# Kernel optimization log

Measured on AMD Instinct MI355X. Metric: run time of the kernel, lower is better.

## Reference

```python
import jax, jax.numpy as jnp
import numpy as np

NUM_HEADS = 4
LN_EPS = 1e-5


def setup_inputs() -> dict:
    key = jax.random.key(0)
    B, S, D = 4, 2048, 1024
    H = NUM_HEADS
    hd = D // H
    ks = jax.random.split(key, 8)
    s = 1.0 / np.sqrt(hd)
    inp = {
        "embeddings": jax.random.normal(ks[0], (B, S, D), dtype=jnp.float32),
        # per-head Q/K/V projection weights (torch Linear weight layout [out,in])
        "Wq": jax.random.normal(ks[1], (H, hd, hd), dtype=jnp.float32) * s,
        "Wk": jax.random.normal(ks[2], (H, hd, hd), dtype=jnp.float32) * s,
        "Wv": jax.random.normal(ks[3], (H, hd, hd), dtype=jnp.float32) * s,
        # lens bias scalars: causal, intent, temporal, normative (init values from module)
        "bias_scalars": jnp.array([0.1, 0.15, 0.05, 0.2], dtype=jnp.float32),
        "Wo_w": jax.random.normal(ks[4], (D, D), dtype=jnp.float32) / np.sqrt(D),
        "Wo_b": jnp.zeros((D,), dtype=jnp.float32),
        "ln_g": jnp.ones((D,), dtype=jnp.float32),
        "ln_b": jnp.zeros((D,), dtype=jnp.float32),
    }
    return inp


def _legal_biases(x, bias_scalars):
    """x: [B,H,S,hd] per-head embeddings. Returns stacked bias [B,H,S,S]."""
    B, H, S, hd = x.shape
    # head 0: CAUSAL -> strictly upper triangular mask * causal_bias
    causal = jnp.triu(jnp.ones((S, S), dtype=x.dtype), k=1)  # [S,S]
    b0 = causal[None] * bias_scalars[0]                      # [1,S,S] -> bcast B
    b0 = jnp.broadcast_to(b0, (B, S, S))
    # head 1: INTENTIONALITY -> outer product of embedding norms, global-mean threshold
    mag1 = jnp.linalg.norm(x[:, 1], axis=-1)                 # [B,S]
    intent = mag1[:, :, None] * mag1[:, None, :]             # [B,S,S]
    b1 = (intent > intent.mean()).astype(x.dtype) * bias_scalars[1]
    # head 2: TEMPORAL -> exp(-|i-j|/S)
    pos = jnp.arange(S, dtype=x.dtype)
    prox = jnp.exp(-jnp.abs(pos[:, None] - pos[None, :]) / S)  # [S,S]
    b2 = jnp.broadcast_to(prox[None] * bias_scalars[2], (B, S, S))
    # head 3: NORMATIVE -> outer product of last feature, > 0.5 threshold
    v3 = x[:, 3, :, -1]                                      # [B,S]
    viol = v3[:, :, None] * v3[:, None, :]                   # [B,S,S]
    b3 = (viol > 0.5).astype(x.dtype) * bias_scalars[3]
    return jnp.stack([b0, b1, b2, b3], axis=1)               # [B,H,S,S]


def _forward(embeddings, Wq, Wk, Wv, bias_scalars, Wo_w, Wo_b, ln_g, ln_b):
    B, S, D = embeddings.shape
    H = NUM_HEADS
    hd = D // H
    x = embeddings.reshape(B, S, H, hd).transpose(0, 2, 1, 3)     # [B,H,S,hd]
    # torch Linear: y = x @ W.T
    Q = jnp.einsum('bhsd,hed->bhse', x, Wq)
    K = jnp.einsum('bhsd,hed->bhse', x, Wk)
    V = jnp.einsum('bhsd,hed->bhse', x, Wv)
    scores = jnp.einsum('bhse,bhte->bhst', Q, K) / np.sqrt(hd)    # [B,H,S,S]
    scores = scores + _legal_biases(x, bias_scalars)
    weights = jax.nn.softmax(scores, axis=-1)                     # [B,H,S,S]
    attended = jnp.einsum('bhst,bhte->bhse', weights, V)          # [B,H,S,hd]
    concat = attended.transpose(0, 2, 1, 3).reshape(B, S, D)      # head order = concat order
    out = concat @ Wo_w.T + Wo_b
    # layer_norm(out + embeddings)
    y = out + embeddings
    mu = y.mean(axis=-1, keepdims=True)
    var = ((y - mu) ** 2).mean(axis=-1, keepdims=True)
    output = (y - mu) / jnp.sqrt(var + LN_EPS) * ln_g + ln_b      # [B,S,D]
    average_weights = weights.mean(axis=1)                        # [B,S,S]
    guilt = jax.nn.softmax(average_weights.sum(axis=-1), axis=-1) # [B,S]
    return output, average_weights, guilt


def reference(embeddings, Wq, Wk, Wv, bias_scalars, Wo_w, Wo_b, ln_g, ln_b):
    return _forward(embeddings, Wq, Wk, Wv, bias_scalars, Wo_w, Wo_b, ln_g, ln_b)
```

## Files before the change

kernel.cpp:

```cpp
#include <hip/hip_runtime.h>
#include <hip/hip_bf16.h>
#include <math.h>

#define S_ 2048
#define D_ 1024
#define H_ 4
#define HD_ 256
#define B_ 4

typedef __hip_bfloat16 bf16;
typedef short s16x8 __attribute__((ext_vector_type(8)));
typedef float f32x4 __attribute__((ext_vector_type(4)));

#define GLOAD16(g, l)                                             \
    __builtin_amdgcn_global_load_lds(                             \
        (const __attribute__((address_space(1))) void*)(g),       \
        (__attribute__((address_space(3))) void*)(l), 16, 0, 0)


template <int MODE>
__global__ __launch_bounds__(256) void mfma_nt(
    int K,
    const bf16* __restrict__ A, int lda, long sA_b, long sA_h,
    const bf16* __restrict__ Bm, int ldb, long sB_b, long sB_h,
    void* __restrict__ Cp, int ldc, long sC_b, long sC_h,
    int zdiv, int bbase,
    const double* __restrict__ mag1d, const double* __restrict__ v3d,
    const double* __restrict__ meand, const float* __restrict__ bias_sc)
{
    __shared__ __align__(16) short As[128 * 32];
    __shared__ __align__(16) short Bs[128 * 32];

    const int tid = threadIdx.x;
    const int w = tid >> 6, lane = tid & 63;
    const int srow = lane >> 2;
    const int scol = (((lane & 3) ^ (srow & 3)) << 3);
    const int quad = lane >> 4, r = lane & 15;
    const int qx = quad ^ (r & 3);
    const int wr = (w >> 1) * 64, wc = (w & 1) * 64;
    const int zb = blockIdx.z / zdiv, zh = blockIdx.z % zdiv;

    const bf16* Ap = A + (size_t)zb * sA_b + (size_t)zh * sA_h +
                     (size_t)blockIdx.y * 128 * lda;
    const bf16* Bp = Bm + (size_t)zb * sB_b + (size_t)zh * sB_h +
                     (size_t)blockIdx.x * 128 * ldb;

    f32x4 acc[4][4] = {};

    for (int k0 = 0; k0 < K; k0 += 32) {
        if (k0) __syncthreads();
#pragma unroll
        for (int l = 0; l < 2; l++) {
            GLOAD16(Ap + (size_t)(w * 32 + l * 16 + srow) * lda + (k0 + scol),
                    &As[(w * 32 + l * 16) * 32]);
            GLOAD16(Bp + (size_t)(w * 32 + l * 16 + srow) * ldb + (k0 + scol),
                    &Bs[(w * 32 + l * 16) * 32]);
        }
        __syncthreads();

        s16x8 af[4], bfv[4];
        const s16x8* A8 = (const s16x8*)As;
        const s16x8* B8 = (const s16x8*)Bs;
#pragma unroll
        for (int i = 0; i < 4; i++) af[i] = A8[(wr + i * 16 + r) * 4 + qx];
#pragma unroll
        for (int j = 0; j < 4; j++) bfv[j] = B8[(wc + j * 16 + r) * 4 + qx];
#pragma unroll
        for (int i = 0; i < 4; i++)
#pragma unroll
            for (int j = 0; j < 4; j++)
                acc[i][j] = __builtin_amdgcn_mfma_f32_16x16x32_bf16(
                    af[i], bfv[j], acc[i][j], 0, 0, 0);
    }

    const int row0 = blockIdx.y * 128 + wr + quad * 4;
    const int col0 = blockIdx.x * 128 + wc + r;

    if (MODE == 0) {
        float* C = (float*)Cp + (size_t)zb * sC_b + (size_t)zh * sC_h;
#pragma unroll
        for (int i = 0; i < 4; i++)
#pragma unroll
            for (int j = 0; j < 4; j++)
#pragma unroll
                for (int p = 0; p < 4; p++)
                    C[(size_t)(row0 + i * 16 + p) * ldc + (col0 + j * 16)] = acc[i][j][p];
    } else if (MODE == 1) {
        bf16* C = (bf16*)Cp + (size_t)zb * sC_b + (size_t)zh * sC_h;
#pragma unroll
        for (int i = 0; i < 4; i++)
#pragma unroll
            for (int j = 0; j < 4; j++)
#pragma unroll
                for (int p = 0; p < 4; p++)
                    C[(size_t)(row0 + i * 16 + p) * ldc + (col0 + j * 16)] =
                        __float2bfloat16(acc[i][j][p]);
    } else {
        float* C = (float*)Cp + (size_t)zb * sC_b + (size_t)zh * sC_h;
        const int h = zh;
        const int bbatch = bbase + zb;
        const float bsc = bias_sc[h];
        if (h == 0) {
#pragma unroll
            for (int i = 0; i < 4; i++)
#pragma unroll
                for (int j = 0; j < 4; j++)
#pragma unroll
                    for (int p = 0; p < 4; p++) {
                        const int rr = row0 + i * 16 + p, c = col0 + j * 16;
                        C[(size_t)rr * ldc + c] = acc[i][j][p] + ((c > rr) ? bsc : 0.0f);
                    }
        } else if (h == 2) {
#pragma unroll
            for (int i = 0; i < 4; i++)
#pragma unroll
                for (int j = 0; j < 4; j++)
#pragma unroll
                    for (int p = 0; p < 4; p++) {
                        const int rr = row0 + i * 16 + p, c = col0 + j * 16;
                        int d = c - rr; d = d < 0 ? -d : d;
                        C[(size_t)rr * ldc + c] =
                            acc[i][j][p] + bsc * expf(-(float)d * (1.0f / 2048.0f));
                    }
        } else {
            const double* src = (h == 1) ? mag1d : v3d;
            const double thr = (h == 1) ? meand[0] : 0.5;
            double rv[16], cv[4];
#pragma unroll
            for (int i = 0; i < 4; i++)
#pragma unroll
                for (int p = 0; p < 4; p++)
                    rv[i * 4 + p] = src[(size_t)bbatch * S_ + row0 + i * 16 + p];
#pragma unroll
            for (int j = 0; j < 4; j++)
                cv[j] = src[(size_t)bbatch * S_ + col0 + j * 16];
#pragma unroll
            for (int i = 0; i < 4; i++)
#pragma unroll
                for (int j = 0; j < 4; j++)
#pragma unroll
                    for (int p = 0; p < 4; p++) {
                        const int rr = row0 + i * 16 + p, c = col0 + j * 16;
                        C[(size_t)rr * ldc + c] =
                            acc[i][j][p] + ((rv[i * 4 + p] * cv[j] > thr) ? bsc : 0.0f);
                    }
        }
    }
}

__global__ __launch_bounds__(512) void mfma_pv(const bf16* __restrict__ Pm,
                                               const bf16* __restrict__ Vt,
                                               bf16* __restrict__ Cc) {
    __shared__ __align__(16) short L[6][12288];

    const int tid = threadIdx.x;
    const int w = tid >> 6, lane = tid & 63;
    const int quad = lane >> 4, r = lane & 15;
    const int qx = quad ^ (r & 3);
    const int wr = (w >> 2) * 64, wc = (w & 3) * 64;

    const int bid = blockIdx.x;
    const int bh = (bid & 7) * 2 + ((bid >> 3) >> 4);
    const int rb = (bid >> 3) & 15;
    const int b = bh >> 2, h = bh & 3;

    const bf16* Ap = Pm + ((size_t)bh * S_ + (size_t)rb * 128) * S_;
    const bf16* Bp = Vt + (size_t)(h * B_ + b) * HD_ * S_;

    const int srow = tid >> 2;
    const int scol = (((tid & 3) ^ (srow & 3)) << 3);
    const int wbase = w * 512;

    f32x4 acc[4][4] = {};

    auto stage = [&](int bs, int t) {
        short* sb = &L[bs][0];
        const int k0 = t * 32;
        GLOAD16(Ap + (size_t)srow * S_ + (k0 + scol), sb + wbase);
        GLOAD16(Bp + (size_t)srow * S_ + (k0 + scol), sb + 4096 + wbase);
        GLOAD16(Bp + (size_t)(128 + srow) * S_ + (k0 + scol), sb + 8192 + wbase);
    };
    auto compute = [&](int bs) {
        const s16x8* A8 = (const s16x8*)&L[bs][0];
        const s16x8* B8 = (const s16x8*)&L[bs][4096];
        s16x8 af[4], bfv[4];
#pragma unroll
        for (int i = 0; i < 4; i++) af[i] = A8[(wr + i * 16 + r) * 4 + qx];
#pragma unroll
        for (int j = 0; j < 4; j++) bfv[j] = B8[(wc + j * 16 + r) * 4 + qx];
        __builtin_amdgcn_s_setprio(1);
#pragma unroll
        for (int i = 0; i < 4; i++)
#pragma unroll
            for (int j = 0; j < 4; j++)
                acc[i][j] = __builtin_amdgcn_mfma_f32_16x16x32_bf16(
                    af[i], bfv[j], acc[i][j], 0, 0, 0);
        __builtin_amdgcn_s_setprio(0);
    };

#define PV_WAITB(N)                                           \
    asm volatile("s_waitcnt vmcnt(" #N ")" ::: "memory");     \
    __builtin_amdgcn_s_barrier();                             \
    __builtin_amdgcn_sched_barrier(0);

    stage(0, 0); stage(1, 1); stage(2, 2); stage(3, 3); stage(4, 4);

    int cb = 0, sn = 5;
#pragma unroll 1
    for (int t = 0; t < 59; ++t) {
        PV_WAITB(12);
        stage(sn, t + 5);
        compute(cb);
        cb = (cb == 5) ? 0 : cb + 1;
        sn = (sn == 5) ? 0 : sn + 1;
    }
    PV_WAITB(12); compute(cb); cb = (cb == 5) ? 0 : cb + 1;
    PV_WAITB(9);  compute(cb); cb = (cb == 5) ? 0 : cb + 1;
    PV_WAITB(6);  compute(cb); cb = (cb == 5) ? 0 : cb + 1;
    PV_WAITB(3);  compute(cb); cb = (cb == 5) ? 0 : cb + 1;
    PV_WAITB(0);  compute(cb);
#undef PV_WAITB

    const int row0 = rb * 128 + wr + quad * 4;
    const int col0 = h * HD_ + wc + r;
    bf16* C = Cc + (size_t)b * S_ * D_;
#pragma unroll
    for (int i = 0; i < 4; i++)
#pragma unroll
        for (int j = 0; j < 4; j++)
#pragma unroll
            for (int p = 0; p < 4; p++)
                C[(size_t)(row0 + i * 16 + p) * D_ + col0 + j * 16] =
                    __float2bfloat16(acc[i][j][p]);
}

__global__ __launch_bounds__(256) void cvt_bf16(const float* __restrict__ in,
                                                bf16* __restrict__ out, int n,
                                                float scale) {
    const size_t i0 = ((size_t)blockIdx.x * 256 + threadIdx.x) * 4;
    if (i0 + 3 < (size_t)n) {
        const float4 v = *(const float4*)(in + i0);
        out[i0 + 0] = __float2bfloat16(v.x * scale);
        out[i0 + 1] = __float2bfloat16(v.y * scale);
        out[i0 + 2] = __float2bfloat16(v.z * scale);
        out[i0 + 3] = __float2bfloat16(v.w * scale);
    }
}

__global__ __launch_bounds__(256) void transpose_v(const bf16* __restrict__ in,
                                                   bf16* __restrict__ out) {
    const int h = blockIdx.z / B_, b = blockIdx.z % B_;
    const int e0 = blockIdx.x * 64, s0 = blockIdx.y * 64;
    __shared__ short t[64][66];
    const int tid = threadIdx.x;
    const int rr = tid >> 2;
    const int cc = (tid & 3) << 4;
    const bf16* ip = in + (((size_t)h * B_ * S_) + (size_t)b * S_ + s0) * HD_ + e0;
    const s16x8 v0 = *(const s16x8*)(ip + (size_t)rr * HD_ + cc);
    const s16x8 v1 = *(const s16x8*)(ip + (size_t)rr * HD_ + cc + 8);
#pragma unroll
    for (int i = 0; i < 8; i++) {
        t[rr][cc + i] = v0[i];
        t[rr][cc + 8 + i] = v1[i];
    }
    __syncthreads();
    bf16* op = out + (((size_t)h * B_ + b) * HD_ + e0 + rr) * S_ + s0 + cc;
    s16x8 o0, o1;
#pragma unroll
    for (int i = 0; i < 8; i++) {
        o0[i] = t[cc + i][rr];
        o1[i] = t[cc + 8 + i][rr];
    }
    *(s16x8*)op = o0;
    *(s16x8*)(op + 8) = o1;
}

__global__ __launch_bounds__(256) void prep_kernel(const float* __restrict__ emb,
                                                   double* __restrict__ mag1d,
                                                   double* __restrict__ v3d) {
    const long row = blockIdx.x;
    const int tid = threadIdx.x;
    const float x = emb[row * D_ + 256 + tid];
    __shared__ double red[256];
    red[tid] = (double)x * (double)x;
    __syncthreads();
    for (int off = 128; off > 0; off >>= 1) {
        if (tid < off) red[tid] += red[tid + off];
        __syncthreads();
    }
    if (tid == 0) {
        mag1d[row] = sqrt(red[0]);
        v3d[row] = (double)emb[row * D_ + 1023];
    }
}

__global__ __launch_bounds__(256) void mean_kernel(const double* __restrict__ mag1d,
                                                   double* __restrict__ meand) {
    const int tid = threadIdx.x;
    __shared__ double red[256];
    double acc = 0.0;
    for (int b = 0; b < B_; b++) {
        double ss = 0.0;
        for (int i = tid; i < S_; i += 256) ss += mag1d[(long)b * S_ + i];
        __syncthreads();
        red[tid] = ss;
        __syncthreads();
        for (int off = 128; off > 0; off >>= 1) {
            if (tid < off) red[tid] += red[tid + off];
            __syncthreads();
        }
        if (tid == 0) {
            const double rb = red[0] / (double)S_;
            acc += rb * rb;
        }
        __syncthreads();
    }
    if (tid == 0) meand[0] = acc / (double)B_;
}

__global__ __launch_bounds__(256) void softmax_fused(
    const float* __restrict__ scores, bf16* __restrict__ P, long p_h, int p_row,
    float* __restrict__ avgw, float* __restrict__ rowsum) {
    const int s = blockIdx.x, tid = threadIdx.x;
    __shared__ float red[256];
    float wacc[8] = {0, 0, 0, 0, 0, 0, 0, 0};
    for (int h = 0; h < H_; h++) {
        const float* rp = scores + ((size_t)h * S_ + s) * S_;
        bf16* pp = P + (size_t)h * p_h + (size_t)s * p_row;
        float v[8];
        float m = -1e30f;
#pragma unroll
        for (int i = 0; i < 8; i++) {
            v[i] = rp[tid + 256 * i];
            m = fmaxf(m, v[i]);
        }
        red[tid] = m;
        __syncthreads();
        for (int off = 128; off > 0; off >>= 1) {
            if (tid < off) red[tid] = fmaxf(red[tid], red[tid + off]);
            __syncthreads();
        }
        m = red[0];
        __syncthreads();
        float sum = 0.0f;
#pragma unroll
        for (int i = 0; i < 8; i++) {
            v[i] = expf(v[i] - m);
            sum += v[i];
        }
        red[tid] = sum;
        __syncthreads();
        for (int off = 128; off > 0; off >>= 1) {
            if (tid < off) red[tid] += red[tid + off];
            __syncthreads();
        }
        const float inv = 1.0f / red[0];
        __syncthreads();
#pragma unroll
        for (int i = 0; i < 8; i++) {
            const float wv = v[i] * inv;
            pp[tid + 256 * i] = __float2bfloat16(wv);
            wacc[i] += wv;
        }
    }
    float asum = 0.0f;
#pragma unroll
    for (int i = 0; i < 8; i++) {
        const float a = wacc[i] * 0.25f;
        avgw[(size_t)s * S_ + tid + 256 * i] = a;
        asum += a;
    }
    red[tid] = asum;
    __syncthreads();
    for (int off = 128; off > 0; off >>= 1) {
        if (tid < off) red[tid] += red[tid + off];
        __syncthreads();
    }
    if (tid == 0) rowsum[s] = red[0];
}

__global__ __launch_bounds__(256) void ln_kernel(float* __restrict__ out,
                                                 const float* __restrict__ emb,
                                                 const float* __restrict__ wob,
                                                 const float* __restrict__ g,
                                                 const float* __restrict__ beta) {
    const long row = blockIdx.x;
    float* o = out + row * D_;
    const float* e = emb + row * D_;
    const int tid = threadIdx.x;
    __shared__ float red[256];
    float v[4];
    float sum = 0.0f;
#pragma unroll
    for (int i = 0; i < 4; i++) {
        const int c = tid + 256 * i;
        v[i] = o[c] + wob[c] + e[c];
        sum += v[i];
    }
    red[tid] = sum;
    __syncthreads();
    for (int off = 128; off > 0; off >>= 1) {
        if (tid < off) red[tid] += red[tid + off];
        __syncthreads();
    }
    const float mu = red[0] * (1.0f / 1024.0f);
    __syncthreads();
    float vs = 0.0f;
#pragma unroll
    for (int i = 0; i < 4; i++) {
        const float d = v[i] - mu;
        vs += d * d;
    }
    red[tid] = vs;
    __syncthreads();
    for (int off = 128; off > 0; off >>= 1) {
        if (tid < off) red[tid] += red[tid + off];
        __syncthreads();
    }
    const float var = red[0] * (1.0f / 1024.0f);
    const float inv = 1.0f / sqrtf(var + 1e-5f);
#pragma unroll
    for (int i = 0; i < 4; i++) {
        const int c = tid + 256 * i;
        o[c] = (v[i] - mu) * inv * g[c] + beta[c];
    }
}

__global__ __launch_bounds__(256) void guilt_kernel(const float* __restrict__ rowsum,
                                                    float* __restrict__ guilt) {
    const int b = blockIdx.x, tid = threadIdx.x;
    const float* r = rowsum + (long)b * S_;
    float* gq = guilt + (long)b * S_;
    __shared__ float red[256];
    float v[8];
    float m = -1e30f;
#pragma unroll
    for (int i = 0; i < 8; i++) {
        v[i] = r[tid + 256 * i];
        m = fmaxf(m, v[i]);
    }
    red[tid] = m;
    __syncthreads();
    for (int off = 128; off > 0; off >>= 1) {
        if (tid < off) red[tid] = fmaxf(red[tid], red[tid + off]);
        __syncthreads();
    }
    m = red[0];
    __syncthreads();
    float sum = 0.0f;
#pragma unroll
    for (int i = 0; i < 8; i++) {
        v[i] = expf(v[i] - m);
        sum += v[i];
    }
    red[tid] = sum;
    __syncthreads();
    for (int off = 128; off > 0; off >>= 1) {
        if (tid < off) red[tid] += red[tid + off];
        __syncthreads();
    }
    const float inv = 1.0f / red[0];
#pragma unroll
    for (int i = 0; i < 8; i++) gq[tid + 256 * i] = v[i] * inv;
}

extern "C" void kernel_launch(void* const* d_in, const int* in_sizes, int n_in,
                              void* d_out, int out_size, void* d_ws, size_t ws_size,
                              hipStream_t stream) {
    const float* emb = (const float*)d_in[0];
    const float* Wq = (const float*)d_in[1];
    const float* Wk = (const float*)d_in[2];
    const float* Wv = (const float*)d_in[3];
    const float* bias_sc = (const float*)d_in[4];
    const float* Wo_w = (const float*)d_in[5];
    const float* Wo_b = (const float*)d_in[6];
    const float* ln_g = (const float*)d_in[7];
    const float* ln_bt = (const float*)d_in[8];

    char* ws = (char*)d_ws;
    size_t off = 0;
    auto alloc = [&](size_t bytes) {
        size_t o = off;
        off = (off + bytes + 255) & ~(size_t)255;
        return o;
    };
    bf16* embb = (bf16*)(ws + alloc((size_t)B_ * S_ * D_ * 2));
    bf16* concat = embb;
    bf16* Qm = (bf16*)(ws + alloc((size_t)H_ * B_ * S_ * HD_ * 2));
    bf16* Km = (bf16*)(ws + alloc((size_t)H_ * B_ * S_ * HD_ * 2));
    bf16* Vtb = (bf16*)(ws + alloc((size_t)H_ * B_ * HD_ * S_ * 2));
    bf16* Wqb = (bf16*)(ws + alloc((size_t)H_ * HD_ * HD_ * 2));
    bf16* Wkb = (bf16*)(ws + alloc((size_t)H_ * HD_ * HD_ * 2));
    bf16* Wvb = (bf16*)(ws + alloc((size_t)H_ * HD_ * HD_ * 2));
    bf16* Wob = (bf16*)(ws + alloc((size_t)D_ * D_ * 2));
    double* mag1d = (double*)(ws + alloc((size_t)B_ * S_ * 8));
    double* v3d = (double*)(ws + alloc((size_t)B_ * S_ * 8));
    double* meand = (double*)(ws + alloc(256));
    float* rowsum = (float*)(ws + alloc((size_t)B_ * S_ * 4));
    float* scores = (float*)(ws + alloc((size_t)H_ * S_ * S_ * 4));
    bf16* Vraw = (bf16*)scores;
    bf16* P = (bf16*)(ws + off);
    const size_t need_batched = off + (size_t)B_ * H_ * S_ * S_ * 2;
    const bool batched = ws_size >= need_batched;

    float* outp = (float*)d_out;
    float* avgw = outp + (size_t)B_ * S_ * D_;
    float* guilt = avgw + (size_t)B_ * S_ * S_;

    cvt_bf16<<<(B_ * S_ * D_) / 1024, 256, 0, stream>>>(emb, embb, B_ * S_ * D_, 1.0f);
    cvt_bf16<<<(H_ * HD_ * HD_) / 1024, 256, 0, stream>>>(Wq, Wqb, H_ * HD_ * HD_, 0.0625f);
    cvt_bf16<<<(H_ * HD_ * HD_) / 1024, 256, 0, stream>>>(Wk, Wkb, H_ * HD_ * HD_, 1.0f);
    cvt_bf16<<<(H_ * HD_ * HD_) / 1024, 256, 0, stream>>>(Wv, Wvb, H_ * HD_ * HD_, 1.0f);
    cvt_bf16<<<(D_ * D_) / 1024, 256, 0, stream>>>(Wo_w, Wob, D_ * D_, 1.0f);

    prep_kernel<<<B_ * S_, 256, 0, stream>>>(emb, mag1d, v3d);
    mean_kernel<<<1, 256, 0, stream>>>(mag1d, meand);

    {
        const dim3 g(HD_ / 128, (B_ * S_) / 128, H_);
        const long sQ = (long)B_ * S_ * HD_;
        mfma_nt<1><<<g, 256, 0, stream>>>(HD_, embb, D_, 0, HD_,
                                          Wqb, HD_, 0, (long)HD_ * HD_,
                                          Qm, HD_, 0, sQ, H_, 0,
                                          nullptr, nullptr, nullptr, nullptr);
        mfma_nt<1><<<g, 256, 0, stream>>>(HD_, embb, D_, 0, HD_,
                                          Wkb, HD_, 0, (long)HD_ * HD_,
                                          Km, HD_, 0, sQ, H_, 0,
                                          nullptr, nullptr, nullptr, nullptr);
        mfma_nt<1><<<g, 256, 0, stream>>>(HD_, embb, D_, 0, HD_,
                                          Wvb, HD_, 0, (long)HD_ * HD_,
                                          Vraw, HD_, 0, sQ, H_, 0,
                                          nullptr, nullptr, nullptr, nullptr);
    }
    transpose_v<<<dim3(HD_ / 64, S_ / 64, H_ * B_), 256, 0, stream>>>(Vraw, Vtb);

    for (int b = 0; b < B_; b++) {
        mfma_nt<3><<<dim3(S_ / 128, S_ / 128, H_), 256, 0, stream>>>(
            HD_,
            Qm + (size_t)b * S_ * HD_, HD_, 0, (long)B_ * S_ * HD_,
            Km + (size_t)b * S_ * HD_, HD_, 0, (long)B_ * S_ * HD_,
            scores, S_, 0, (long)S_ * S_,
            H_, b, mag1d, v3d, meand, bias_sc);
        if (batched) {
            softmax_fused<<<S_, 256, 0, stream>>>(
                scores, P + (size_t)b * H_ * S_ * S_, (long)S_ * S_, S_,
                avgw + (size_t)b * S_ * S_, rowsum + (size_t)b * S_);
        } else {
            softmax_fused<<<S_, 256, 0, stream>>>(
                scores, (bf16*)scores, 2L * S_ * S_, 2 * S_,
                avgw + (size_t)b * S_ * S_, rowsum + (size_t)b * S_);
            mfma_nt<1><<<dim3(HD_ / 128, S_ / 128, H_), 256, 0, stream>>>(
                S_,
                (const bf16*)scores, 2 * S_, 0, 2L * S_ * S_,
                Vtb + (size_t)b * HD_ * S_, S_, 0, (long)B_ * HD_ * S_,
                concat + (size_t)b * S_ * D_, D_, 0, HD_,
                H_, 0, nullptr, nullptr, nullptr, nullptr);
        }
    }
    if (batched) {
        mfma_pv<<<256, 512, 0, stream>>>(P, Vtb, concat);
    }

    mfma_nt<0><<<dim3(D_ / 128, (B_ * S_) / 128, 1), 256, 0, stream>>>(
        D_, concat, D_, 0, 0, Wob, D_, 0, 0, outp, D_, 0, 0,
        1, 0, nullptr, nullptr, nullptr, nullptr);

    ln_kernel<<<B_ * S_, 256, 0, stream>>>(outp, emb, Wo_b, ln_g, ln_bt);
    guilt_kernel<<<B_, 256, 0, stream>>>(rowsum, guilt);
}
```

Before: 509.2 us.

## Retile PV GEMM to 64-row blocks of 256 threads with triple buffering

Result: slower. 524.3 us (+3.0%).

```diff
diff --git a/kernel.cpp b/kernel.cpp
--- a/kernel.cpp
+++ b/kernel.cpp
@@ -148,44 +148,46 @@
     }
 }
 
-__global__ __launch_bounds__(512) void mfma_pv(const bf16* __restrict__ Pm,
+__global__ __launch_bounds__(256) void mfma_pv(const bf16* __restrict__ Pm,
                                                const bf16* __restrict__ Vt,
                                                bf16* __restrict__ Cc) {
-    __shared__ __align__(16) short L[6][12288];
+    __shared__ __align__(16) short L[3 * 10240];
 
     const int tid = threadIdx.x;
     const int w = tid >> 6, lane = tid & 63;
     const int quad = lane >> 4, r = lane & 15;
     const int qx = quad ^ (r & 3);
-    const int wr = (w >> 2) * 64, wc = (w & 3) * 64;
+    const int wc = w * 64;
 
     const int bid = blockIdx.x;
-    const int bh = (bid & 7) * 2 + ((bid >> 3) >> 4);
-    const int rb = (bid >> 3) & 15;
+    const int idx = bid >> 3;
+    const int bh = (bid & 7) * 2 + (idx >> 5);
+    const int rb = idx & 31;
     const int b = bh >> 2, h = bh & 3;
 
-    const bf16* Ap = Pm + ((size_t)bh * S_ + (size_t)rb * 128) * S_;
+    const bf16* Ap = Pm + ((size_t)bh * S_ + (size_t)rb * 64) * S_;
     const bf16* Bp = Vt + (size_t)(h * B_ + b) * HD_ * S_;
 
     const int srow = tid >> 2;
     const int scol = (((tid & 3) ^ (srow & 3)) << 3);
-    const int wbase = w * 512;
 
     f32x4 acc[4][4] = {};
 
     auto stage = [&](int bs, int t) {
-        short* sb = &L[bs][0];
+        short* sb = &L[bs * 10240];
         const int k0 = t * 32;
-        GLOAD16(Ap + (size_t)srow * S_ + (k0 + scol), sb + wbase);
-        GLOAD16(Bp + (size_t)srow * S_ + (k0 + scol), sb + 4096 + wbase);
-        GLOAD16(Bp + (size_t)(128 + srow) * S_ + (k0 + scol), sb + 8192 + wbase);
+        GLOAD16(Ap + (size_t)srow * S_ + (k0 + scol), sb + w * 512);
+#pragma unroll
+        for (int l = 0; l < 4; l++)
+            GLOAD16(Bp + (size_t)(l * 64 + srow) * S_ + (k0 + scol),
+                    sb + 2048 + l * 2048 + w * 512);
     };
     auto compute = [&](int bs) {
-        const s16x8* A8 = (const s16x8*)&L[bs][0];
-        const s16x8* B8 = (const s16x8*)&L[bs][4096];
+        const s16x8* A8 = (const s16x8*)&L[bs * 10240];
+        const s16x8* B8 = (const s16x8*)&L[bs * 10240 + 2048];
         s16x8 af[4], bfv[4];
 #pragma unroll
-        for (int i = 0; i < 4; i++) af[i] = A8[(wr + i * 16 + r) * 4 + qx];
+        for (int i = 0; i < 4; i++) af[i] = A8[(i * 16 + r) * 4 + qx];
 #pragma unroll
         for (int j = 0; j < 4; j++) bfv[j] = B8[(wc + j * 16 + r) * 4 + qx];
         __builtin_amdgcn_s_setprio(1);
@@ -203,25 +205,22 @@
     __builtin_amdgcn_s_barrier();                             \
     __builtin_amdgcn_sched_barrier(0);
 
-    stage(0, 0); stage(1, 1); stage(2, 2); stage(3, 3); stage(4, 4);
-
-    int cb = 0, sn = 5;
+    stage(0, 0); stage(1, 1);
+
+    int cb = 0;
 #pragma unroll 1
-    for (int t = 0; t < 59; ++t) {
-        PV_WAITB(12);
-        stage(sn, t + 5);
+    for (int t = 0; t < 62; ++t) {
+        PV_WAITB(5);
+        int sb_i = cb + 2; if (sb_i >= 3) sb_i -= 3;
+        stage(sb_i, t + 2);
         compute(cb);
-        cb = (cb == 5) ? 0 : cb + 1;
-        sn = (sn == 5) ? 0 : sn + 1;
-    }
-    PV_WAITB(12); compute(cb); cb = (cb == 5) ? 0 : cb + 1;
-    PV_WAITB(9);  compute(cb); cb = (cb == 5) ? 0 : cb + 1;
-    PV_WAITB(6);  compute(cb); cb = (cb == 5) ? 0 : cb + 1;
-    PV_WAITB(3);  compute(cb); cb = (cb == 5) ? 0 : cb + 1;
+        cb = (cb == 2) ? 0 : cb + 1;
+    }
+    PV_WAITB(5);  compute(cb); cb = (cb == 2) ? 0 : cb + 1;
     PV_WAITB(0);  compute(cb);
 #undef PV_WAITB
 
-    const int row0 = rb * 128 + wr + quad * 4;
+    const int row0 = rb * 64 + quad * 4;
     const int col0 = h * HD_ + wc + r;
     bf16* C = Cc + (size_t)b * S_ * D_;
 #pragma unroll
@@ -558,7 +557,7 @@
         }
     }
     if (batched) {
-        mfma_pv<<<256, 512, 0, stream>>>(P, Vtb, concat);
+        mfma_pv<<<512, 256, 0, stream>>>(P, Vtb, concat);
     }
 
     mfma_nt<0><<<dim3(D_ / 128, (B_ * S_) / 128, 1), 256, 0, stream>>>(
```
